# Kernel tuning notes

Hardware: AMD Instinct MI355X
Metric: run time of the kernel (lower is better)

## Reference

```python
import jax, jax.numpy as jnp
import numpy as np

HH, WW = 56, 56          # input resolution
WS, SS = 7, 3            # window size, shift size
HEADS = 6
DIM = 192
HID = 768
B = 32
EPS = 1e-5


def _rel_pos_index(ws):
    coords = np.stack(np.meshgrid(np.arange(ws), np.arange(ws), indexing='ij'))  # [2,ws,ws]
    cf = coords.reshape(2, -1)                       # [2,N]
    rel = cf[:, :, None] - cf[:, None, :]            # [2,N,N]
    rel = rel.transpose(1, 2, 0).copy()              # [N,N,2]
    rel[:, :, 0] += ws - 1
    rel[:, :, 1] += ws - 1
    rel[:, :, 0] *= 2 * ws - 1
    return rel.sum(-1)                               # [N,N] int


def _attn_mask(H, W, ws, ss):
    img = np.zeros((H, W))
    cnt = 0
    sl = (slice(0, -ws), slice(-ws, -ss), slice(-ss, None))
    for hs in sl:
        for wsl in sl:
            img[hs, wsl] = cnt
            cnt += 1
    mw = img.reshape(H // ws, ws, W // ws, ws).transpose(0, 2, 1, 3).reshape(-1, ws * ws)  # [nW,N]
    diff = mw[:, None, :] - mw[:, :, None]           # matches unsqueeze(1)-unsqueeze(2)
    return np.where(diff != 0, -100.0, 0.0).astype(np.float32)  # [nW,N,N]


_RPI = jnp.asarray(_rel_pos_index(WS))               # [49,49] int
_MASK = jnp.asarray(_attn_mask(HH, WW, WS, SS))      # [64,49,49] f32


def _ln(v, g, b):
    mu = v.mean(-1, keepdims=True)
    var = v.var(-1, keepdims=True)
    return (v - mu) / jnp.sqrt(var + EPS) * g + b


def setup_inputs() -> dict:
    key = jax.random.key(0)
    ks = jax.random.split(key, 10)
    s = 0.02
    return {
        'x': jax.random.normal(ks[0], (B, HH * WW, DIM), jnp.float32),
        'norm1_g': jnp.ones((DIM,), jnp.float32),
        'norm1_b': jnp.zeros((DIM,), jnp.float32),
        'qkv_w': jax.random.normal(ks[1], (DIM, 3 * DIM), jnp.float32) * s,
        'qkv_b': jax.random.normal(ks[2], (3 * DIM,), jnp.float32) * s,
        'rpb_table': jax.random.normal(ks[3], (169, HEADS), jnp.float32) * s,
        'proj_w': jax.random.normal(ks[4], (DIM, DIM), jnp.float32) * s,
        'proj_b': jax.random.normal(ks[5], (DIM,), jnp.float32) * s,
        'norm2_g': jnp.ones((DIM,), jnp.float32),
        'norm2_b': jnp.zeros((DIM,), jnp.float32),
        'fc1_w': jax.random.normal(ks[6], (DIM, HID), jnp.float32) * s,
        'fc1_b': jax.random.normal(ks[7], (HID,), jnp.float32) * s,
        'fc2_w': jax.random.normal(ks[8], (HID, DIM), jnp.float32) * s,
        'fc2_b': jax.random.normal(ks[9], (DIM,), jnp.float32) * s,
    }


def reference(x, norm1_g, norm1_b, qkv_w, qkv_b, rpb_table, proj_w, proj_b,
              norm2_g, norm2_b, fc1_w, fc1_b, fc2_w, fc2_b):
    Bn, L, C = x.shape
    h, ws, ss = HEADS, WS, SS
    d = C // h
    scale = d ** -0.5
    N = ws * ws
    nWh, nWw = HH // ws, WW // ws

    shortcut = x
    xh = _ln(x, norm1_g, norm1_b).reshape(Bn, HH, WW, C)
    xh = jnp.roll(xh, (-ss, -ss), axis=(1, 2))                       # cyclic shift
    # window partition -> (B*nW, N, C)
    xw = xh.reshape(Bn, nWh, ws, nWw, ws, C).transpose(0, 1, 3, 2, 4, 5).reshape(-1, N, C)

    qkv = (xw @ qkv_w + qkv_b).reshape(-1, N, 3, h, d).transpose(2, 0, 3, 1, 4)
    q, k, v = qkv[0] * scale, qkv[1], qkv[2]                         # (B_,h,N,d)
    attn = jnp.einsum('bhnd,bhmd->bhnm', q, k)                       # (B_,h,N,N)

    bias = rpb_table[_RPI.reshape(-1)].reshape(N, N, h).transpose(2, 0, 1)  # (h,N,N)
    attn = attn + bias[None]
    nW = _MASK.shape[0]
    attn = attn.reshape(Bn, nW, h, N, N) + _MASK[None, :, None]
    attn = jax.nn.softmax(attn.reshape(-1, h, N, N), axis=-1)

    out = jnp.einsum('bhnm,bhmd->bhnd', attn, v).transpose(0, 2, 1, 3).reshape(-1, N, C)
    out = out @ proj_w + proj_b
    # window reverse
    out = out.reshape(Bn, nWh, nWw, ws, ws, C).transpose(0, 1, 3, 2, 4, 5).reshape(Bn, HH, WW, C)
    out = jnp.roll(out, (ss, ss), axis=(1, 2)).reshape(Bn, L, C)     # reverse shift

    x1 = shortcut + out
    y = _ln(x1, norm2_g, norm2_b)
    y = jax.nn.gelu(y @ fc1_w + fc1_b, approximate=False)
    y = y @ fc2_w + fc2_b
    return x1 + y
```

## Files before the change

### kernel.cpp

```cpp
#include <hip/hip_runtime.h>
#include <cmath>

typedef __bf16  v8bf  __attribute__((ext_vector_type(8)));
typedef float   v4f   __attribute__((ext_vector_type(4)));

#define HH 56
#define WW2 56
#define SS 3
#define HEADS 6
#define DIM 192
#define HID 768
#define NTOK 49
#define NWIN 2048
#define MTOT (NWIN * NTOK)
#define SCALE 0.17677669529663687f

__device__ __forceinline__ void async_cp16(const __bf16* g, __bf16* l) {
    __builtin_amdgcn_global_load_lds(
        (const __attribute__((address_space(1))) void*)g,
        (__attribute__((address_space(3))) void*)l,
        16, 0, 0);
}

__device__ __forceinline__ void wg_barrier() {
    __builtin_amdgcn_sched_barrier(0);
    __builtin_amdgcn_s_barrier();
    __builtin_amdgcn_sched_barrier(0);
}
#define WAIT_LGKM0() asm volatile("s_waitcnt lgkmcnt(0)" ::: "memory")
#define WAIT_VM(n)   asm volatile("s_waitcnt vmcnt(" #n ")" ::: "memory")

__device__ __forceinline__ float fast_gelu(float x) {
    float z = fabsf(x) * 0.70710678118654752f;
    float t = __builtin_amdgcn_rcpf(1.f + 0.3275911f * z);
    float poly = t * (0.254829592f + t * (-0.284496736f +
                 t * (1.421413741f + t * (-1.453152027f + t * 1.061405429f))));
    float er = 1.f - poly * __expf(-z * z);
    er = (x < 0.f) ? -er : er;
    return 0.5f * x * (1.f + er);
}

__global__ void k_transpose(const float* __restrict__ in, __bf16* __restrict__ out,
                            int K, int N) {
    int idx = blockIdx.x * 256 + threadIdx.x;
    if (idx >= K * N) return;
    int n = idx / K, k = idx - n * K;
    out[idx] = (__bf16)in[k * N + n];
}

__global__ void k_prep_fc1(const float* __restrict__ w, __bf16* __restrict__ o) {
    int idx = blockIdx.x * 256 + threadIdx.x;
    if (idx >= HID * DIM) return;
    int n = idx / DIM, rem = idx - n * DIM;
    int b16 = rem >> 3, j = rem & 7;
    int k = 8 * (b16 ^ (n & 7)) + j;
    o[idx] = (__bf16)w[k * HID + n];
}

__global__ void k_prep_fc2(const float* __restrict__ w, __bf16* __restrict__ o) {
    int idx = blockIdx.x * 256 + threadIdx.x;
    if (idx >= HID * DIM) return;
    int hc = idx / (DIM * 64);
    int rem = idx - hc * DIM * 64;
    int n = rem >> 6;
    int rem2 = rem & 63;
    int b16 = rem2 >> 3, j = rem2 & 7;
    int k = hc * 64 + 8 * (b16 ^ (n & 7)) + j;
    o[idx] = (__bf16)w[k * DIM + n];
}

__global__ void k_bias(const float* __restrict__ rpb, float* __restrict__ bt) {
    int type = blockIdx.x, h = blockIdx.y;
    for (int idx = threadIdx.x; idx < 4096; idx += 256) {
        int m = idx >> 6, n = idx & 63;
        float v;
        if (m >= 49) v = -1e9f;
        else if (n >= 49) v = 0.f;
        else {
            int ni = n / 7, nj = n % 7, mi = m / 7, mj = m % 7;
            v = rpb[((ni - mi + 6) * 13 + (nj - mj + 6)) * 6 + h];
            int rin = (type & 2) ? ((ni < 4) ? 1 : 2) : 0;
            int rjn = (type & 1) ? ((nj < 4) ? 1 : 2) : 0;
            int rim = (type & 2) ? ((mi < 4) ? 1 : 2) : 0;
            int rjm = (type & 1) ? ((mj < 4) ? 1 : 2) : 0;
            if (rin * 3 + rjn != rim * 3 + rjm) v -= 100.f;
        }
        bt[((size_t)(type * HEADS + h) * 64 + m) * 64 + n] = v;
    }
}

__global__ __launch_bounds__(256) void k_ln1win(const float* __restrict__ x,
                                                const float* __restrict__ g,
                                                const float* __restrict__ bt,
                                                __bf16* __restrict__ xw) {
    int wv = threadIdx.x >> 6, lane = threadIdx.x & 63;
    int t = blockIdx.x * 4 + wv;
    int w = t / NTOK, p = t - w * NTOK;
    int b = w >> 6, wi = w & 63;
    int i = (wi >> 3) * 7 + p / 7;
    int j = (wi & 7) * 7 + p % 7;
    int io = i + SS; if (io >= HH) io -= HH;
    int jo = j + SS; if (jo >= WW2) jo -= WW2;
    const float* src = x + ((size_t)(b * 3136 + io * 56 + jo)) * DIM;
    float v0 = src[lane], v1 = src[lane + 64], v2 = src[lane + 128];
    float s = v0 + v1 + v2, s2 = v0 * v0 + v1 * v1 + v2 * v2;
    #pragma unroll
    for (int off = 1; off < 64; off <<= 1) {
        s  += __shfl_xor(s, off);
        s2 += __shfl_xor(s2, off);
    }
    float mu = s * (1.f / 192.f);
    float rstd = rsqrtf(s2 * (1.f / 192.f) - mu * mu + 1e-5f);
    __bf16* dst = xw + (size_t)t * DIM;
    dst[lane]       = (__bf16)((v0 - mu) * rstd * g[lane]       + bt[lane]);
    dst[lane + 64]  = (__bf16)((v1 - mu) * rstd * g[lane + 64]  + bt[lane + 64]);
    dst[lane + 128] = (__bf16)((v2 - mu) * rstd * g[lane + 128] + bt[lane + 128]);
}

template<int KDIM, int NDIM, int MODE>
__global__ __launch_bounds__(256) void k_gemm128(const __bf16* __restrict__ A,
                                                 const __bf16* __restrict__ Wt,
                                                 const float* __restrict__ bias,
                                                 __bf16* __restrict__ outb,
                                                 const float* __restrict__ x1in,
                                                 float* __restrict__ outf,
                                                 const float* __restrict__ xres) {
    __shared__ __bf16 lA[128 * 32];
    __shared__ __bf16 lB[128 * 32];
    const int tid = threadIdx.x;
    const int m0 = blockIdx.x * 128, n0 = blockIdx.y * 128;
    const int wv = tid >> 6, lane = tid & 63;
    const int wm = (wv >> 1) * 64, wn = (wv & 1) * 64;
    const int lrow = lane & 15, lq = lane >> 4;
    const int grow = tid >> 2, gkc = (tid & 3) * 8;
    v4f acc[4][4] = {};
    for (int kk = 0; kk < KDIM; kk += 32) {
        #pragma unroll
        for (int c = 0; c < 2; c++) {
            int r = grow + c * 64;
            async_cp16(A + (size_t)(m0 + r) * KDIM + kk + gkc, lA + tid * 8 + c * 2048);
            int rb = n0 + r;
            if (NDIM % 128) rb = (rb < NDIM) ? rb : (NDIM - 1);
            async_cp16(Wt + (size_t)rb * KDIM + kk + gkc, lB + tid * 8 + c * 2048);
        }
        __syncthreads();
        v8bf af[4], bf[4];
        #pragma unroll
        for (int i = 0; i < 4; i++) {
            af[i] = *(const v8bf*)(lA + (wm + i * 16 + lrow) * 32 + lq * 8);
            bf[i] = *(const v8bf*)(lB + (wn + i * 16 + lrow) * 32 + lq * 8);
        }
        #pragma unroll
        for (int i = 0; i < 4; i++)
        #pragma unroll
        for (int j = 0; j < 4; j++)
            acc[i][j] = __builtin_amdgcn_mfma_f32_16x16x32_bf16(af[i], bf[j], acc[i][j], 0, 0, 0);
        __syncthreads();
    }
    #pragma unroll
    for (int i = 0; i < 4; i++)
    #pragma unroll
    for (int j = 0; j < 4; j++) {
        int col = n0 + wn + j * 16 + lrow;
        if (NDIM % 128 && col >= NDIM) continue;
        float bv = bias[col];
        #pragma unroll
        for (int r = 0; r < 4; r++) {
            int row = m0 + wm + i * 16 + lq * 4 + r;
            float v = acc[i][j][r] + bv;
            if (MODE == 0) {
                __bf16* kbp = outb + (size_t)MTOT * DIM;
                __bf16* vbp = kbp + (size_t)MTOT * DIM;
                int which = col / DIM, rem = col - which * DIM;
                int hh = rem >> 5, d = rem & 31;
                int w = row / NTOK, p = row - w * NTOK;
                size_t off = ((size_t)(w * HEADS + hh) * NTOK + p) * 32 + d;
                if (which == 0)      outb[off] = (__bf16)(v * SCALE);
                else if (which == 1) kbp[off] = (__bf16)v;
                else                 vbp[off] = (__bf16)v;
            } else {
                int w = row / NTOK, p = row - w * NTOK;
                int bimg = w >> 6, wi = w & 63;
                int ii = (wi >> 3) * 7 + p / 7;
                int jj = (wi & 7) * 7 + p % 7;
                int io = ii + SS; if (io >= HH) io -= HH;
                int jo = jj + SS; if (jo >= WW2) jo -= WW2;
                size_t o = ((size_t)(bimg * 3136 + io * 56 + jo)) * DIM + col;
                outf[o] = v + xres[o];
            }
        }
    }
}

__global__ __launch_bounds__(64) void k_attn_mfma(const __bf16* __restrict__ qb,
                                                  const float* __restrict__ bias_tab,
                                                  __bf16* __restrict__ ao) {
    __shared__ __bf16 Pl[64 * 72];
    __shared__ __bf16 VTl[32 * 72];
    const __bf16* kb = qb + (size_t)MTOT * DIM;
    const __bf16* vb = kb + (size_t)MTOT * DIM;
    int wh = blockIdx.x;
    int w = wh / HEADS, h = wh - w * HEADS;
    int lane = threadIdx.x & 63;
    int c = lane & 15, q = lane >> 4;
    const size_t base = (size_t)wh * (NTOK * 32);

    for (int idx = lane; idx < 32 * 16; idx += 64)
        VTl[(idx >> 4) * 72 + 48 + (idx & 15)] = (__bf16)0.f;
    #pragma unroll
    for (int it = 0; it < 4; it++) {
        int idx = it * 64 + lane;
        if (idx < NTOK * 4) {
            int t = idx >> 2, d0 = (idx & 3) * 8;
            v8bf vv = *(const v8bf*)(vb + base + t * 32 + d0);
            #pragma unroll
            for (int ii = 0; ii < 8; ii++) VTl[(d0 + ii) * 72 + t] = vv[ii];
        }
    }
    v8bf af[4], bf[4];
    #pragma unroll
    for (int rt = 0; rt < 4; rt++) {
        int t = rt * 16 + c; t = (t > 48) ? 48 : t;
        af[rt] = *(const v8bf*)(qb + base + t * 32 + q * 8);
        bf[rt] = *(const v8bf*)(kb + base + t * 32 + q * 8);
    }
    v4f S[4][4] = {};
    #pragma unroll
    for (int rt = 0; rt < 4; rt++)
    #pragma unroll
    for (int ct = 0; ct < 4; ct++)
        S[rt][ct] = __builtin_amdgcn_mfma_f32_16x16x32_bf16(af[rt], bf[ct], S[rt][ct], 0, 0, 0);
    int wi = w & 63;
    int type = (((wi >> 3) == 7) ? 2 : 0) + (((wi & 7) == 7) ? 1 : 0);
    const float* bt = bias_tab + (size_t)(type * HEADS + h) * 4096;
    #pragma unroll
    for (int rt = 0; rt < 4; rt++)
    #pragma unroll
    for (int ct = 0; ct < 4; ct++) {
        v4f bv = *(const v4f*)(bt + (ct * 16 + c) * 64 + rt * 16 + q * 4);
        S[rt][ct] += bv;
    }
    v4f mx4[4], inv4[4];
    #pragma unroll
    for (int rt = 0; rt < 4; rt++) {
        v4f m;
        #pragma unroll
        for (int r = 0; r < 4; r++)
            m[r] = fmaxf(fmaxf(S[rt][0][r], S[rt][1][r]), fmaxf(S[rt][2][r], S[rt][3][r]));
        #pragma unroll
        for (int off = 1; off < 16; off <<= 1) {
            #pragma unroll
            for (int r = 0; r < 4; r++) m[r] = fmaxf(m[r], __shfl_xor(m[r], off));
        }
        mx4[rt] = m;
    }
    #pragma unroll
    for (int rt = 0; rt < 4; rt++) {
        v4f dsum = {};
        #pragma unroll
        for (int ct = 0; ct < 4; ct++) {
            #pragma unroll
            for (int r = 0; r < 4; r++) {
                float e = __expf(S[rt][ct][r] - mx4[rt][r]);
                dsum[r] += e;
                Pl[(rt * 16 + q * 4 + r) * 72 + ct * 16 + c] = (__bf16)e;
            }
        }
        #pragma unroll
        for (int off = 1; off < 16; off <<= 1) {
            #pragma unroll
            for (int r = 0; r < 4; r++) dsum[r] += __shfl_xor(dsum[r], off);
        }
        #pragma unroll
        for (int r = 0; r < 4; r++) inv4[rt][r] = 1.f / dsum[r];
    }
    __syncthreads();
    v4f O[4][2] = {};
    #pragma unroll
    for (int k2 = 0; k2 < 2; k2++) {
        v8bf pa[4], pb[2];
        #pragma unroll
        for (int rt = 0; rt < 4; rt++)
            pa[rt] = *(const v8bf*)(Pl + (rt * 16 + c) * 72 + k2 * 32 + q * 8);
        #pragma unroll
        for (int ct = 0; ct < 2; ct++)
            pb[ct] = *(const v8bf*)(VTl + (ct * 16 + c) * 72 + k2 * 32 + q * 8);
        #pragma unroll
        for (int rt = 0; rt < 4; rt++)
        #pragma unroll
        for (int ct = 0; ct < 2; ct++)
            O[rt][ct] = __builtin_amdgcn_mfma_f32_16x16x32_bf16(pa[rt], pb[ct], O[rt][ct], 0, 0, 0);
    }
    __bf16* aop = ao + (size_t)(w * NTOK) * DIM + h * 32;
    #pragma unroll
    for (int rt = 0; rt < 4; rt++)
    #pragma unroll
    for (int r = 0; r < 4; r++) {
        int row = rt * 16 + q * 4 + r;
        if (row < NTOK) {
            #pragma unroll
            for (int ct = 0; ct < 2; ct++)
                aop[(size_t)row * DIM + ct * 16 + c] = (__bf16)(O[rt][ct][r] * inv4[rt][r]);
        }
    }
}

__global__ __launch_bounds__(256, 2) void k_mlp_fused(
        const float* __restrict__ x1,
        const float* __restrict__ n2g, const float* __restrict__ n2b,
        const __bf16* __restrict__ fc1S, const float* __restrict__ fc1b,
        const __bf16* __restrict__ fc2S, const float* __restrict__ fc2b,
        float* __restrict__ out) {
    __shared__ __align__(16) char sm[61184];
    char* bufX = sm;
    char* bufY = sm + 24576;
    char* lH   = sm + 49152;
    float* lB1 = (float*)(sm + 57344);
    float* lB2 = (float*)(sm + 60416);
    const int tid = threadIdx.x;
    const int wv = tid >> 6, lane = tid & 63;
    const int lrow = lane & 15, lq = lane >> 4;
    const int m0 = blockIdx.x * 64;

    #pragma unroll
    for (int p = 0; p < 6; ++p)
        async_cp16(fc1S + p * 2048 + tid * 8, (__bf16*)bufY + p * 2048 + tid * 8);

    #pragma unroll
    for (int p = 0; p < 3; ++p) lB1[p * 256 + tid] = fc1b[p * 256 + tid];
    if (tid < 192) lB2[tid] = fc2b[tid];

    {
        float g0 = n2g[lane], g1 = n2g[lane + 64], g2 = n2g[lane + 128];
        float b0 = n2b[lane], b1 = n2b[lane + 64], b2 = n2b[lane + 128];
        #pragma unroll 4
        for (int it = 0; it < 16; ++it) {
            int row = wv * 16 + it;
            const float* src = x1 + (size_t)(m0 + row) * DIM;
            float v0 = src[lane], v1 = src[lane + 64], v2 = src[lane + 128];
            float s = v0 + v1 + v2, s2 = v0 * v0 + v1 * v1 + v2 * v2;
            #pragma unroll
            for (int off = 1; off < 64; off <<= 1) {
                s  += __shfl_xor(s, off);
                s2 += __shfl_xor(s2, off);
            }
            float mu = s * (1.f / 192.f);
            float rstd = rsqrtf(s2 * (1.f / 192.f) - mu * mu + 1e-5f);
            char* rb = bufX + row * 384;
            int xo = (row & 7) << 4;
            *(__bf16*)(rb + ((lane * 2)       ^ xo)) = (__bf16)((v0 - mu) * rstd * g0 + b0);
            *(__bf16*)(rb + ((lane * 2 + 128) ^ xo)) = (__bf16)((v1 - mu) * rstd * g1 + b1);
            *(__bf16*)(rb + ((lane * 2 + 256) ^ xo)) = (__bf16)((v2 - mu) * rstd * g2 + b2);
        }
    }
    WAIT_LGKM0();
    wg_barrier();

    const int wm  = (wv >> 1) * 32;
    const int wc1 = (wv & 1) * 32;
    const int wn  = (wv & 1) * 96;
    v8bf afr[2][6];
    #pragma unroll
    for (int i = 0; i < 2; ++i) {
        int ra = wm + i * 16 + lrow;
        #pragma unroll
        for (int ks = 0; ks < 6; ++ks)
            afr[i][ks] = *(const v8bf*)(bufX + ra * 384 + ((ks * 64 + lq * 16) ^ ((ra & 7) << 4)));
    }
    WAIT_LGKM0();
    wg_barrier();

    #pragma unroll
    for (int p = 0; p < 6; ++p)
        async_cp16(fc2S + p * 2048 + tid * 8, (__bf16*)bufX + p * 2048 + tid * 8);

    v4f oacc[2][6] = {};
    for (int hc = 0; hc < 12; ++hc) {
        int hn = hc + 1; if (hn == 12) hn = 0;
        v4f hacc[2][2] = {};
        __builtin_amdgcn_s_setprio(1);
        #pragma unroll
        for (int ks = 0; ks < 6; ++ks) {
            v8bf bw[2];
            #pragma unroll
            for (int j = 0; j < 2; ++j) {
                int rw = wc1 + j * 16 + lrow;
                bw[j] = *(const v8bf*)(bufY + rw * 384 + ((ks * 64 + lq * 16) ^ ((rw & 7) << 4)));
            }
            #pragma unroll
            for (int i = 0; i < 2; ++i)
            #pragma unroll
            for (int j = 0; j < 2; ++j)
                hacc[i][j] = __builtin_amdgcn_mfma_f32_16x16x32_bf16(afr[i][ks], bw[j], hacc[i][j], 0, 0, 0);
        }
        __builtin_amdgcn_s_setprio(0);
        #pragma unroll
        for (int i = 0; i < 2; ++i)
        #pragma unroll
        for (int j = 0; j < 2; ++j) {
            float bv = lB1[hc * 64 + wc1 + j * 16 + lrow];
            #pragma unroll
            for (int r = 0; r < 4; ++r) {
                int row = wm + i * 16 + lq * 4 + r;
                int col = wc1 + j * 16 + lrow;
                float hv = hacc[i][j][r] + bv;
                *(__bf16*)(lH + row * 128 + ((col * 2) ^ ((row & 7) << 4))) = (__bf16)fast_gelu(hv);
            }
        }
        WAIT_LGKM0();
        wg_barrier();
        {
            const __bf16* s1 = fc1S + (size_t)hn * (64 * 192);
            #pragma unroll
            for (int p = 0; p < 6; ++p)
                async_cp16(s1 + p * 2048 + tid * 8, (__bf16*)bufY + p * 2048 + tid * 8);
        }
        WAIT_VM(6);
        wg_barrier();
        __builtin_amdgcn_s_setprio(1);
        #pragma unroll
        for (int k2 = 0; k2 < 2; ++k2) {
            v8bf pa[2], pb[6];
            #pragma unroll
            for (int i = 0; i < 2; ++i) {
                int ra = wm + i * 16 + lrow;
                pa[i] = *(const v8bf*)(lH + ra * 128 + ((k2 * 64 + lq * 16) ^ ((ra & 7) << 4)));
            }
            #pragma unroll
            for (int j = 0; j < 6; ++j) {
                int rw = wn + j * 16 + lrow;
                pb[j] = *(const v8bf*)(bufX + rw * 128 + ((k2 * 64 + lq * 16) ^ ((rw & 7) << 4)));
            }
            #pragma unroll
            for (int i = 0; i < 2; ++i)
            #pragma unroll
            for (int j = 0; j < 6; ++j)
                oacc[i][j] = __builtin_amdgcn_mfma_f32_16x16x32_bf16(pa[i], pb[j], oacc[i][j], 0, 0, 0);
        }
        __builtin_amdgcn_s_setprio(0);
        WAIT_LGKM0();
        wg_barrier();
        {
            const __bf16* s2 = fc2S + (size_t)hn * (192 * 64);
            #pragma unroll
            for (int p = 0; p < 6; ++p)
                async_cp16(s2 + p * 2048 + tid * 8, (__bf16*)bufX + p * 2048 + tid * 8);
        }
        WAIT_VM(6);
        wg_barrier();
    }
    WAIT_VM(0);
    #pragma unroll
    for (int i = 0; i < 2; ++i)
    #pragma unroll
    for (int j = 0; j < 6; ++j) {
        int col = wn + j * 16 + lrow;
        float bv = lB2[col];
        #pragma unroll
        for (int r = 0; r < 4; ++r) {
            int row = m0 + wm + i * 16 + lq * 4 + r;
            size_t o = (size_t)row * DIM + col;
            out[o] = oacc[i][j][r] + bv + x1[o];
        }
    }
}

extern "C" void kernel_launch(void* const* d_in, const int* in_sizes, int n_in,
                              void* d_out, int out_size, void* d_ws, size_t ws_size,
                              hipStream_t stream) {
    const float* x      = (const float*)d_in[0];
    const float* n1g    = (const float*)d_in[1];
    const float* n1b    = (const float*)d_in[2];
    const float* qkv_w  = (const float*)d_in[3];
    const float* qkv_b  = (const float*)d_in[4];
    const float* rpb    = (const float*)d_in[5];
    const float* proj_w = (const float*)d_in[6];
    const float* proj_b = (const float*)d_in[7];
    const float* n2g    = (const float*)d_in[8];
    const float* n2b    = (const float*)d_in[9];
    const float* fc1_w  = (const float*)d_in[10];
    const float* fc1_b  = (const float*)d_in[11];
    const float* fc2_w  = (const float*)d_in[12];
    const float* fc2_b  = (const float*)d_in[13];
    float* outp = (float*)d_out;

    char* ws = (char*)d_ws;
    const size_t SZA = (size_t)MTOT * DIM * 2;
    __bf16* xw = (__bf16*)ws;
    __bf16* qb = (__bf16*)(ws + SZA);
    float*  x1 = (float*)(ws + SZA);
    char* wbase = ws + 4 * SZA;
    __bf16* qkvT  = (__bf16*)wbase;
    __bf16* projT = qkvT + 576 * 192;
    __bf16* fc1S  = projT + 192 * 192;
    __bf16* fc2S  = fc1S + 768 * 192;
    float*  btab  = (float*)(fc2S + 768 * 192);

    k_transpose<<<(192 * 576 + 255) / 256, 256, 0, stream>>>(qkv_w, qkvT, 192, 576);
    k_transpose<<<(192 * 192 + 255) / 256, 256, 0, stream>>>(proj_w, projT, 192, 192);
    k_prep_fc1<<<(768 * 192 + 255) / 256, 256, 0, stream>>>(fc1_w, fc1S);
    k_prep_fc2<<<(768 * 192 + 255) / 256, 256, 0, stream>>>(fc2_w, fc2S);
    k_bias<<<dim3(4, HEADS), 256, 0, stream>>>(rpb, btab);

    k_ln1win<<<MTOT / 4, 256, 0, stream>>>(x, n1g, n1b, xw);

    k_gemm128<192, 576, 0><<<dim3(MTOT / 128, 5), 256, 0, stream>>>(
        xw, qkvT, qkv_b, qb, nullptr, nullptr, nullptr);

    k_attn_mfma<<<NWIN * HEADS, 64, 0, stream>>>(qb, btab, xw);

    k_gemm128<192, 192, 1><<<dim3(MTOT / 128, 2), 256, 0, stream>>>(
        xw, projT, proj_b, nullptr, nullptr, x1, x);

    k_mlp_fused<<<MTOT / 64, 256, 0, stream>>>(
        x1, n2g, n2b, fc1S, fc1_b, fc2S, fc2_b, outp);
}
```

Measured before the change: 477.8 us.

## Double-buffer GEMM LDS loads and halve MLP hidden chunk for higher occupancy

The generic 128x128 GEMM now uses two LDS buffers. The next k-slice is prefetched while the current one feeds MFMA, which replaces the load, sync, compute, sync sequence. The fused MLP kernel processes the hidden dimension in 32-wide chunks instead of 64-wide. This cuts LDS use from about 61KB to 40KB, so launch bounds rise from 2 to 4 blocks per CU, and the fc2 weight prep layout changes to match. The cost is twice as many chunk iterations with their barriers, and smaller MFMA batches per chunk. The fc2 and hidden tiles also drop their swizzle and may hit bank conflicts.

```diff
diff --git a/kernel.cpp b/kernel.cpp
--- a/kernel.cpp
+++ b/kernel.cpp
@@ -60,13 +60,10 @@
 __global__ void k_prep_fc2(const float* __restrict__ w, __bf16* __restrict__ o) {
     int idx = blockIdx.x * 256 + threadIdx.x;
     if (idx >= HID * DIM) return;
-    int hc = idx / (DIM * 64);
-    int rem = idx - hc * DIM * 64;
-    int n = rem >> 6;
-    int rem2 = rem & 63;
-    int b16 = rem2 >> 3, j = rem2 & 7;
-    int k = hc * 64 + 8 * (b16 ^ (n & 7)) + j;
-    o[idx] = (__bf16)w[k * DIM + n];
+    int hc = idx / (192 * 32);
+    int rem = idx - hc * 192 * 32;
+    int n = rem >> 5, k = rem & 31;
+    o[idx] = (__bf16)w[(hc * 32 + k) * DIM + n];
 }
 
 __global__ void k_bias(const float* __restrict__ rpb, float* __restrict__ bt) {
@@ -125,37 +122,47 @@
                                                  const float* __restrict__ x1in,
                                                  float* __restrict__ outf,
                                                  const float* __restrict__ xres) {
-    __shared__ __bf16 lA[128 * 32];
-    __shared__ __bf16 lB[128 * 32];
+    __shared__ __bf16 lA[2][128 * 32];
+    __shared__ __bf16 lB[2][128 * 32];
     const int tid = threadIdx.x;
     const int m0 = blockIdx.x * 128, n0 = blockIdx.y * 128;
     const int wv = tid >> 6, lane = tid & 63;
     const int wm = (wv >> 1) * 64, wn = (wv & 1) * 64;
     const int lrow = lane & 15, lq = lane >> 4;
     const int grow = tid >> 2, gkc = (tid & 3) * 8;
-    v4f acc[4][4] = {};
-    for (int kk = 0; kk < KDIM; kk += 32) {
+
+    auto stage = [&](int kk, int b) {
         #pragma unroll
         for (int c = 0; c < 2; c++) {
             int r = grow + c * 64;
-            async_cp16(A + (size_t)(m0 + r) * KDIM + kk + gkc, lA + tid * 8 + c * 2048);
+            async_cp16(A + (size_t)(m0 + r) * KDIM + kk + gkc, lA[b] + tid * 8 + c * 2048);
             int rb = n0 + r;
             if (NDIM % 128) rb = (rb < NDIM) ? rb : (NDIM - 1);
-            async_cp16(Wt + (size_t)rb * KDIM + kk + gkc, lB + tid * 8 + c * 2048);
-        }
-        __syncthreads();
+            async_cp16(Wt + (size_t)rb * KDIM + kk + gkc, lB[b] + tid * 8 + c * 2048);
+        }
+    };
+    stage(0, 0);
+    stage(32, 1);
+
+    v4f acc[4][4] = {};
+    #pragma unroll
+    for (int kk = 0; kk < KDIM; kk += 32) {
+        const int b = (kk >> 5) & 1;
+        if (kk + 32 < KDIM) { WAIT_VM(4); } else { WAIT_VM(0); }
+        wg_barrier();
         v8bf af[4], bf[4];
         #pragma unroll
         for (int i = 0; i < 4; i++) {
-            af[i] = *(const v8bf*)(lA + (wm + i * 16 + lrow) * 32 + lq * 8);
-            bf[i] = *(const v8bf*)(lB + (wn + i * 16 + lrow) * 32 + lq * 8);
+            af[i] = *(const v8bf*)(lA[b] + (wm + i * 16 + lrow) * 32 + lq * 8);
+            bf[i] = *(const v8bf*)(lB[b] + (wn + i * 16 + lrow) * 32 + lq * 8);
         }
         #pragma unroll
         for (int i = 0; i < 4; i++)
         #pragma unroll
         for (int j = 0; j < 4; j++)
             acc[i][j] = __builtin_amdgcn_mfma_f32_16x16x32_bf16(af[i], bf[j], acc[i][j], 0, 0, 0);
-        __syncthreads();
+        wg_barrier();
+        if (kk + 64 < KDIM) stage(kk + 64, b);
     }
     #pragma unroll
     for (int i = 0; i < 4; i++)
@@ -305,25 +312,25 @@
     }
 }
 
-__global__ __launch_bounds__(256, 2) void k_mlp_fused(
+__global__ __launch_bounds__(256, 4) void k_mlp_fused(
         const float* __restrict__ x1,
         const float* __restrict__ n2g, const float* __restrict__ n2b,
         const __bf16* __restrict__ fc1S, const float* __restrict__ fc1b,
         const __bf16* __restrict__ fc2S, const float* __restrict__ fc2b,
         float* __restrict__ out) {
-    __shared__ __align__(16) char sm[61184];
+    __shared__ __align__(16) char sm[40704];
     char* bufX = sm;
+    char* lH   = sm + 12288;
     char* bufY = sm + 24576;
-    char* lH   = sm + 49152;
-    float* lB1 = (float*)(sm + 57344);
-    float* lB2 = (float*)(sm + 60416);
+    float* lB1 = (float*)(sm + 36864);
+    float* lB2 = (float*)(sm + 39936);
     const int tid = threadIdx.x;
     const int wv = tid >> 6, lane = tid & 63;
     const int lrow = lane & 15, lq = lane >> 4;
     const int m0 = blockIdx.x * 64;
 
     #pragma unroll
-    for (int p = 0; p < 6; ++p)
+    for (int p = 0; p < 3; ++p)
         async_cp16(fc1S + p * 2048 + tid * 8, (__bf16*)bufY + p * 2048 + tid * 8);
 
     #pragma unroll
@@ -346,7 +353,7 @@
             }
             float mu = s * (1.f / 192.f);
             float rstd = rsqrtf(s2 * (1.f / 192.f) - mu * mu + 1e-5f);
-            char* rb = bufX + row * 384;
+            char* rb = sm + row * 384;
             int xo = (row & 7) << 4;
             *(__bf16*)(rb + ((lane * 2)       ^ xo)) = (__bf16)((v0 - mu) * rstd * g0 + b0);
             *(__bf16*)(rb + ((lane * 2 + 128) ^ xo)) = (__bf16)((v1 - mu) * rstd * g1 + b1);
@@ -357,7 +364,7 @@
     wg_barrier();
 
     const int wm  = (wv >> 1) * 32;
-    const int wc1 = (wv & 1) * 32;
+    const int wc1 = (wv & 1) * 16;
     const int wn  = (wv & 1) * 96;
     v8bf afr[2][6];
     #pragma unroll
@@ -365,71 +372,63 @@
         int ra = wm + i * 16 + lrow;
         #pragma unroll
         for (int ks = 0; ks < 6; ++ks)
-            afr[i][ks] = *(const v8bf*)(bufX + ra * 384 + ((ks * 64 + lq * 16) ^ ((ra & 7) << 4)));
+            afr[i][ks] = *(const v8bf*)(sm + ra * 384 + ((ks * 64 + lq * 16) ^ ((ra & 7) << 4)));
     }
     WAIT_LGKM0();
     wg_barrier();
 
     #pragma unroll
-    for (int p = 0; p < 6; ++p)
+    for (int p = 0; p < 3; ++p)
         async_cp16(fc2S + p * 2048 + tid * 8, (__bf16*)bufX + p * 2048 + tid * 8);
 
     v4f oacc[2][6] = {};
-    for (int hc = 0; hc < 12; ++hc) {
-        int hn = hc + 1; if (hn == 12) hn = 0;
-        v4f hacc[2][2] = {};
+    for (int hc = 0; hc < 24; ++hc) {
+        int hn = hc + 1; if (hn == 24) hn = 0;
+        v4f hacc[2] = {};
         __builtin_amdgcn_s_setprio(1);
         #pragma unroll
         for (int ks = 0; ks < 6; ++ks) {
-            v8bf bw[2];
-            #pragma unroll
-            for (int j = 0; j < 2; ++j) {
-                int rw = wc1 + j * 16 + lrow;
-                bw[j] = *(const v8bf*)(bufY + rw * 384 + ((ks * 64 + lq * 16) ^ ((rw & 7) << 4)));
-            }
+            int rw = wc1 + lrow;
+            v8bf bw = *(const v8bf*)(bufY + rw * 384 + ((ks * 64 + lq * 16) ^ ((rw & 7) << 4)));
             #pragma unroll
             for (int i = 0; i < 2; ++i)
-            #pragma unroll
-            for (int j = 0; j < 2; ++j)
-                hacc[i][j] = __builtin_amdgcn_mfma_f32_16x16x32_bf16(afr[i][ks], bw[j], hacc[i][j], 0, 0, 0);
+                hacc[i] = __builtin_amdgcn_mfma_f32_16x16x32_bf16(afr[i][ks], bw, hacc[i], 0, 0, 0);
         }
         __builtin_amdgcn_s_setprio(0);
-        #pragma unroll
-        for (int i = 0; i < 2; ++i)
-        #pragma unroll
-        for (int j = 0; j < 2; ++j) {
-            float bv = lB1[hc * 64 + wc1 + j * 16 + lrow];
+        {
+            float bv = lB1[hc * 32 + wc1 + lrow];
+            #pragma unroll
+            for (int i = 0; i < 2; ++i)
             #pragma unroll
             for (int r = 0; r < 4; ++r) {
                 int row = wm + i * 16 + lq * 4 + r;
-                int col = wc1 + j * 16 + lrow;
-                float hv = hacc[i][j][r] + bv;
-                *(__bf16*)(lH + row * 128 + ((col * 2) ^ ((row & 7) << 4))) = (__bf16)fast_gelu(hv);
+                int col = wc1 + lrow;
+                float hv = hacc[i][r] + bv;
+                *(__bf16*)(lH + row * 64 + col * 2) = (__bf16)fast_gelu(hv);
             }
         }
         WAIT_LGKM0();
         wg_barrier();
         {
-            const __bf16* s1 = fc1S + (size_t)hn * (64 * 192);
-            #pragma unroll
-            for (int p = 0; p < 6; ++p)
+            const __bf16* s1 = fc1S + (size_t)hn * (32 * 192);
+            #pragma unroll
+            for (int p = 0; p < 3; ++p)
                 async_cp16(s1 + p * 2048 + tid * 8, (__bf16*)bufY + p * 2048 + tid * 8);
         }
-        WAIT_VM(6);
+        WAIT_VM(3);
         wg_barrier();
         __builtin_amdgcn_s_setprio(1);
-        #pragma unroll
-        for (int k2 = 0; k2 < 2; ++k2) {
+        {
             v8bf pa[2], pb[6];
             #pragma unroll
             for (int i = 0; i < 2; ++i) {
                 int ra = wm + i * 16 + lrow;
-                pa[i] = *(const v8bf*)(lH + ra * 128 + ((k2 * 64 + lq * 16) ^ ((ra & 7) << 4)));
+                pa[i] = *(const v8bf*)(lH + ra * 64 + lq * 16);
             }
             #pragma unroll
             for (int j = 0; j < 6; ++j) {
                 int rw = wn + j * 16 + lrow;
-                pb[j] = *(const v8bf*)(bufX + rw * 128 + ((k2 * 64 + lq * 16) ^ ((rw & 7) << 4)));
+                pb[j] = *(const v8bf*)(bufX + rw * 64 + lq * 16);
             }
             #pragma unroll
             for (int i = 0; i < 2; ++i)
@@ -441,12 +440,12 @@
         WAIT_LGKM0();
         wg_barrier();
         {
-            const __bf16* s2 = fc2S + (size_t)hn * (192 * 64);
-            #pragma unroll
-            for (int p = 0; p < 6; ++p)
+            const __bf16* s2 = fc2S + (size_t)hn * (192 * 32);
+            #pragma unroll
+            for (int p = 0; p < 3; ++p)
                 async_cp16(s2 + p * 2048 + tid * 8, (__bf16*)bufX + p * 2048 + tid * 8);
         }
-        WAIT_VM(6);
+        WAIT_VM(3);
         wg_barrier();
     }
     WAIT_VM(0);
```

Measured after the change: 524.6 us. 9.8% more time.
